# Kernel tuning notes

Hardware: AMD Instinct MI355X
Metric: run time of the kernel (lower is better)

Reference implementation:

```python
import jax, jax.numpy as jnp
import numpy as np

T = 8          # timesteps (init arg)
SCALE = 5.0    # surrogate gradient sharpness (init arg)

# Heaviside spike with sigmoid surrogate gradient (SurrogateSpike.apply equivalent)
@jax.custom_vjp
def spike_fn(mem, thr):
    return (mem >= thr).astype(mem.dtype)

def _spike_fwd(mem, thr):
    return spike_fn(mem, thr), mem - thr  # save delta for backward

def _spike_bwd(delta, g):
    sg = jax.nn.sigmoid(SCALE * delta)
    grad = g * sg * (1.0 - sg) * SCALE
    # threshold grad = -modified_grad, reduced to thr shape (1,)
    return grad, (-jnp.sum(grad)).reshape(1)

spike_fn.defvjp(_spike_fwd, _spike_bwd)


def setup_inputs() -> dict:
    key = jax.random.key(0)
    k1, _ = jax.random.split(key)
    TB, C, H, W = 256, 512, 16, 16  # T*B=256 (B=32)
    x = jax.random.uniform(k1, (TB, C, H, W), dtype=jnp.float32)
    thresh = jnp.array([2.0], dtype=jnp.float32)  # learnable scalar threshold
    return {"x": x, "thresh": thresh}


def reference(x, thresh):
    # ExpandTemporalDim: [T*B, ...] -> [T, B, ...]
    xs = x.reshape(T, x.shape[0] // T, *x.shape[1:])
    mem0 = 0.5 * thresh * jnp.ones_like(xs[0])  # mem init depends on thresh (grad flows)

    def step(mem, xt):
        m = mem + xt                      # integrate
        sb = spike_fn(m, thresh)          # fire (surrogate grad)
        sp = sb * thresh                  # spike scaled by threshold
        return m - sp, sp                 # soft reset

    _, spikes = jax.lax.scan(step, mem0, xs)  # [T, B, ...]
    # MergeTemporalDim: [T, B, ...] -> [T*B, ...]
    return spikes.reshape(x.shape)
```

## Files before the change

### kernel.cpp

```cpp
#include <hip/hip_runtime.h>


typedef float f4 __attribute__((ext_vector_type(4)));

constexpr int T_STEPS = 8;
constexpr int BLOCK   = 256;

__global__ __launch_bounds__(BLOCK, 4) void if_fwd_kernel(
    const f4* __restrict__ x,
    const float* __restrict__ thresh,
    f4* __restrict__ out,
    int stride4)
{
    const int i = blockIdx.x * BLOCK + threadIdx.x;
    if (i >= stride4) return;

    const float thr = thresh[0];
    const float h   = 0.5f * thr;

    f4 xt[T_STEPS];
#pragma unroll
    for (int t = 0; t < T_STEPS; ++t) {
        xt[t] = __builtin_nontemporal_load(x + (size_t)t * stride4 + i);
    }
    __builtin_amdgcn_sched_barrier(0);

    f4 m = {h, h, h, h};
#pragma unroll
    for (int t = 0; t < T_STEPS; ++t) {
        m += xt[t];
        f4 s;
#pragma unroll
        for (int k = 0; k < 4; ++k) {
            s[k] = (m[k] >= thr) ? thr : 0.0f;
        }
        m -= s;
        __builtin_nontemporal_store(s, out + (size_t)t * stride4 + i);
    }
}

extern "C" void kernel_launch(void* const* d_in, const int* in_sizes, int n_in,
                              void* d_out, int out_size, void* d_ws, size_t ws_size,
                              hipStream_t stream) {
    const float* x      = (const float*)d_in[0];
    const float* thresh = (const float*)d_in[1];
    float* out          = (float*)d_out;

    const int total   = in_sizes[0];
    const int stride  = total / T_STEPS;
    const int stride4 = stride / 4;

    dim3 block(BLOCK);
    dim3 grid((stride4 + BLOCK - 1) / BLOCK);
    if_fwd_kernel<<<grid, block, 0, stream>>>(
        (const f4*)x, thresh, (f4*)out, stride4);
}
```

Before: 232.5 us.

## Stage input timesteps into LDS via direct global-to-LDS loads

Input tiles for all 8 timesteps are loaded straight into shared memory with 16-byte global_load_lds transfers, instead of into registers. Each block now covers 512 f4 columns, with each thread doing two columns, and the launch bound drops to 2 blocks per SM. The aim is to issue more loads without register pressure. The cost is 64KB of LDS per block, which limits occupancy, plus a full wait and barrier before any compute or store can start. The bounds check is removed, so the grid assumes the per-timestep size divides evenly by 512.

Result: slower. 246.5 us (+6.0%).

```diff
diff --git a/kernel.cpp b/kernel.cpp
--- a/kernel.cpp
+++ b/kernel.cpp
@@ -5,37 +5,53 @@
 
 constexpr int T_STEPS = 8;
 constexpr int BLOCK   = 256;
+constexpr int R       = 512;
+constexpr int LDS_F4  = T_STEPS * R;
 
-__global__ __launch_bounds__(BLOCK, 4) void if_fwd_kernel(
+__global__ __launch_bounds__(BLOCK, 2) void if_fwd_kernel(
     const f4* __restrict__ x,
     const float* __restrict__ thresh,
     f4* __restrict__ out,
     int stride4)
 {
-    const int i = blockIdx.x * BLOCK + threadIdx.x;
-    if (i >= stride4) return;
+    __shared__ f4 lds[LDS_F4];
+
+    const int tid  = threadIdx.x;
+    const int base = blockIdx.x * R;
 
     const float thr = thresh[0];
     const float h   = 0.5f * thr;
 
-    f4 xt[T_STEPS];
 #pragma unroll
-    for (int t = 0; t < T_STEPS; ++t) {
-        xt[t] = __builtin_nontemporal_load(x + (size_t)t * stride4 + i);
+    for (int j = 0; j < 16; ++j) {
+        const int t = j >> 1;
+        const int r = ((j & 1) << 8) + tid;
+        const f4* src = x + (size_t)t * stride4 + base + r;
+        f4* dst = lds + t * R + r;
+        __builtin_amdgcn_global_load_lds(
+            (const __attribute__((address_space(1))) unsigned int*)src,
+            (__attribute__((address_space(3))) unsigned int*)dst,
+            16 , 0 , 0 );
     }
-    __builtin_amdgcn_sched_barrier(0);
+    __builtin_amdgcn_s_waitcnt(0);
+    __syncthreads();
 
-    f4 m = {h, h, h, h};
 #pragma unroll
-    for (int t = 0; t < T_STEPS; ++t) {
-        m += xt[t];
-        f4 s;
+    for (int half = 0; half < 2; ++half) {
+        const int r = (half << 8) + tid;
+        f4 m = {h, h, h, h};
 #pragma unroll
-        for (int k = 0; k < 4; ++k) {
-            s[k] = (m[k] >= thr) ? thr : 0.0f;
+        for (int t = 0; t < T_STEPS; ++t) {
+            f4 v = lds[t * R + r];
+            m += v;
+            f4 s;
+#pragma unroll
+            for (int k = 0; k < 4; ++k) {
+                s[k] = (m[k] >= thr) ? thr : 0.0f;
+            }
+            m -= s;
+            __builtin_nontemporal_store(s, out + (size_t)t * stride4 + base + r);
         }
-        m -= s;
-        __builtin_nontemporal_store(s, out + (size_t)t * stride4 + i);
     }
 }
 
@@ -51,7 +67,7 @@
     const int stride4 = stride / 4;
 
     dim3 block(BLOCK);
-    dim3 grid((stride4 + BLOCK - 1) / BLOCK);
+    dim3 grid(stride4 / R);
     if_fwd_kernel<<<grid, block, 0, stream>>>(
         (const f4*)x, thresh, (f4*)out, stride4);
 }
```
